# Kernel tuning notes

Hardware: AMD Instinct MI355X
Metric: run time of the kernel (lower is better)

Reference implementation:

```python
import jax, jax.numpy as jnp
import numpy as np

N_NODES = 100000
N_EDGES = 1600000
D = 32
N_GRAPHS = 128


def setup_inputs() -> dict:
    key = jax.random.key(0)
    ks = jax.random.split(key, 6)
    feats = jax.random.normal(ks[0], (N_NODES, D), dtype=jnp.float32)
    src = jax.random.randint(ks[1], (N_EDGES,), 0, N_NODES, dtype=jnp.int32)
    dst = jax.random.randint(ks[2], (N_EDGES,), 0, N_NODES, dtype=jnp.int32)
    graph_ids = jnp.sort(jax.random.randint(ks[3], (N_NODES,), 0, N_GRAPHS, dtype=jnp.int32))
    # Linear weights (torch nn.Linear: y = x @ W.T + b); store as [in, out] here
    W1 = jax.random.normal(ks[4], (D, D), dtype=jnp.float32) * (1.0 / np.sqrt(D))
    b1 = jnp.zeros((D,), dtype=jnp.float32)
    W2 = jax.random.normal(ks[5], (D, D), dtype=jnp.float32) * (1.0 / np.sqrt(D))
    b2 = jnp.zeros((D,), dtype=jnp.float32)
    return {"feats": feats, "src": src, "dst": dst, "graph_ids": graph_ids,
            "W1": W1, "b1": b1, "W2": W2, "b2": b2}


def _gin_conv(x, src, dst, W, b):
    # DGL GINConv, aggregator 'sum', eps=0 (default, non-learnable):
    # h_v = Linear(x_v + sum_{u in N(v)} x_u)
    agg = jax.ops.segment_sum(x[src], dst, num_segments=N_NODES)
    return (x + agg) @ W + b


def reference(feats, src, dst, graph_ids, W1, b1, W2, b2):
    h = _gin_conv(feats, src, dst, W1, b1)          # conv1
    h = jax.nn.relu(h)                               # F.relu
    h = _gin_conv(h, src, dst, W2, b2)               # conv2
    # SumPooling: sum node features per graph -> [N_GRAPHS, D]
    return jax.ops.segment_sum(h, graph_ids, num_segments=N_GRAPHS)
```

## Files before the change

### kernel.cpp

```cpp
#include <hip/hip_runtime.h>
#include <hip/hip_bf16.h>
#include <hip/hip_fp16.h>

#define N_NODES 100000
#define N_EDGES 1600000
#define D 32
#define N_GRAPHS 128

#define WIN 128
#define NWINS ((N_NODES + WIN - 1) / WIN)
#define CAP 2560
#define NODES_PER_WAVE 8

__global__ void bin_kernel(const int* __restrict__ src,
                           const int* __restrict__ dst,
                           int* __restrict__ gfill,
                           int* __restrict__ ebuf) {
    __shared__ int lhist[NWINS];
    __shared__ int lbase[NWINS];
    const int tid = threadIdx.x;
    const int per = (N_EDGES + gridDim.x - 1) / gridDim.x;
    const int e0 = blockIdx.x * per;
    const int e1 = (e0 + per < N_EDGES) ? e0 + per : N_EDGES;

    for (int b = tid; b < NWINS; b += blockDim.x) lhist[b] = 0;
    __syncthreads();
    for (int e = e0 + tid; e < e1; e += blockDim.x)
        atomicAdd(&lhist[dst[e] >> 7], 1);
    __syncthreads();
    for (int b = tid; b < NWINS; b += blockDim.x) {
        int c = lhist[b];
        lbase[b] = c ? atomicAdd(&gfill[b], c) : 0;
        lhist[b] = 0;
    }
    __syncthreads();
    for (int e = e0 + tid; e < e1; e += blockDim.x) {
        int d = dst[e];
        int bn = d >> 7;
        int r = atomicAdd(&lhist[bn], 1);
        int off = lbase[bn] + r;
        if (off < CAP) ebuf[bn * CAP + off] = ((d & (WIN - 1)) << 17) | src[e];
    }
}

__global__ void wscan_kernel(const int* __restrict__ gfill, int* __restrict__ wbase) {
    __shared__ int s[1024];
    const int t = threadIdx.x;
    int v = (t < NWINS) ? gfill[t] : 0;
    s[t] = v;
    __syncthreads();
    for (int off = 1; off < 1024; off <<= 1) {
        int a = (t >= off) ? s[t - off] : 0;
        __syncthreads();
        s[t] += a;
        __syncthreads();
    }
    if (t < NWINS) wbase[t] = s[t] - v;
    if (t == NWINS - 1) wbase[NWINS] = s[t];
}

__global__ void csr_local_kernel(const int* __restrict__ ebuf,
                                 const int* __restrict__ wbase,
                                 int* __restrict__ esrc,
                                 int* __restrict__ rend,
                                 int* __restrict__ deg) {
    __shared__ int pk[CAP];
    __shared__ int ssrc[CAP];
    __shared__ int hs[WIN];
    __shared__ int hcnt[WIN];
    __shared__ int cur[WIN];
    const int tid = threadIdx.x;
    const int w = blockIdx.x;
    const int base_out = wbase[w];
    int cnt = wbase[w + 1] - base_out;
    if (cnt > CAP) cnt = CAP;
    const int n0 = w * WIN;

    for (int i = tid; i < cnt; i += 256) pk[i] = ebuf[w * CAP + i];
    if (tid < WIN) hcnt[tid] = 0;
    __syncthreads();
    for (int i = tid; i < cnt; i += 256) atomicAdd(&hcnt[pk[i] >> 17], 1);
    __syncthreads();
    if (tid < WIN) hs[tid] = hcnt[tid];
    __syncthreads();
    for (int off = 1; off < WIN; off <<= 1) {
        int a = 0;
        if (tid < WIN && tid >= off) a = hs[tid - off];
        __syncthreads();
        if (tid < WIN) hs[tid] += a;
        __syncthreads();
    }
    if (tid < WIN) {
        const int incl = hs[tid];
        const int c = hcnt[tid];
        cur[tid] = incl - c;
        const int n = n0 + tid;
        if (n < N_NODES) { rend[n] = base_out + incl; deg[n] = c; }
    }
    __syncthreads();
    for (int i = tid; i < cnt; i += 256) {
        const int p = pk[i];
        const int pos = atomicAdd(&cur[p >> 17], 1);
        ssrc[pos] = p & 0x1FFFF;
    }
    __syncthreads();
    for (int i = tid; i < cnt; i += 256) esrc[base_out + i] = ssrc[i];
}

__device__ __forceinline__ unsigned pkh2(float a, float b) {
    __half2 h = __floats2half2_rn(a, b);
    return *reinterpret_cast<unsigned*>(&h);
}
__device__ __forceinline__ unsigned hadd2u(unsigned a, unsigned b) {
    __half2 ha = *reinterpret_cast<__half2*>(&a);
    __half2 hb = *reinterpret_cast<__half2*>(&b);
    __half2 r = __hadd2(ha, hb);
    return *reinterpret_cast<unsigned*>(&r);
}
__device__ __forceinline__ float lo2f(unsigned u) { return __low2float(*reinterpret_cast<__half2*>(&u)); }
__device__ __forceinline__ float hi2f(unsigned u) { return __high2float(*reinterpret_cast<__half2*>(&u)); }

__global__ void f32_to_f16_kernel(const float* __restrict__ in, uint4* __restrict__ out) {
    const int i = blockIdx.x * blockDim.x + threadIdx.x;
    if (i >= N_NODES * D / 8) return;
    const float4* p = reinterpret_cast<const float4*>(in) + (size_t)i * 2;
    const float4 v0 = p[0], v1 = p[1];
    uint4 o;
    o.x = pkh2(v0.x, v0.y); o.y = pkh2(v0.z, v0.w);
    o.z = pkh2(v1.x, v1.y); o.w = pkh2(v1.z, v1.w);
    out[i] = o;
}

#define PK_ADD(g) do { \
    acc01 = hadd2u(acc01, (g).x); acc23 = hadd2u(acc23, (g).y); \
    acc45 = hadd2u(acc45, (g).z); acc67 = hadd2u(acc67, (g).w); } while (0)

template <bool RELU, bool POOL>
__global__ void gin_layer_kernel(const uint4* __restrict__ xh,
                                 const int* __restrict__ esrc,
                                 const int* __restrict__ rend,
                                 const int* __restrict__ deg,
                                 const float* __restrict__ W,
                                 const float* __restrict__ bias,
                                 const int* __restrict__ graph_ids,
                                 float* __restrict__ outf,
                                 uint2* __restrict__ outh) {
    const int lane = threadIdx.x & 63;
    const int fq = lane & 3;
    const int es = lane >> 2;
    const int og = lane & 7;
    const int ig = lane >> 3;

    float w[4][4];
#pragma unroll
    for (int k = 0; k < 4; ++k) {
        const float4 t = *reinterpret_cast<const float4*>(&W[(ig * 4 + k) * D + og * 4]);
        w[k][0] = t.x; w[k][1] = t.y; w[k][2] = t.z; w[k][3] = t.w;
    }
    const float4 bv = *reinterpret_cast<const float4*>(&bias[og * 4]);

    const int wid = blockIdx.x * (blockDim.x >> 6) + (threadIdx.x >> 6);
    const int v0 = wid * NODES_PER_WAVE;
    if (v0 >= N_NODES) return;
    const int v1 = (v0 + NODES_PER_WAVE < N_NODES) ? v0 + NODES_PER_WAVE : N_NODES;

    float p0 = 0.f, p1 = 0.f, p2 = 0.f, p3 = 0.f;
    int cur_g = POOL ? graph_ids[v0] : 0;

    for (int v = v0; v < v1; ++v) {
        const int end = rend[v];
        int e = end - deg[v];

        unsigned acc01 = 0u, acc23 = 0u, acc45 = 0u, acc67 = 0u;
        if (es == 0) {
            const uint4 sv = xh[(size_t)v * 4 + fq];
            PK_ADD(sv);
        }

        for (; e + 32 <= end; e += 32) {
            const int r0 = esrc[e + es];
            const int r1 = esrc[e + 16 + es];
            const uint4 g0 = xh[(size_t)r0 * 4 + fq];
            const uint4 g1 = xh[(size_t)r1 * 4 + fq];
            PK_ADD(g0); PK_ADD(g1);
        }
        if (e + 16 <= end) {
            const int r0 = esrc[e + es];
            const uint4 g0 = xh[(size_t)r0 * 4 + fq];
            PK_ADD(g0);
            e += 16;
        }
        const int rem = end - e;
        if (es < rem) {
            const int r0 = esrc[e + es];
            const uint4 g0 = xh[(size_t)r0 * 4 + fq];
            PK_ADD(g0);
        }

#pragma unroll
        for (int off = 4; off <= 32; off <<= 1) {
            acc01 = hadd2u(acc01, (unsigned)__shfl_xor((int)acc01, off));
            acc23 = hadd2u(acc23, (unsigned)__shfl_xor((int)acc23, off));
            acc45 = hadd2u(acc45, (unsigned)__shfl_xor((int)acc45, off));
            acc67 = hadd2u(acc67, (unsigned)__shfl_xor((int)acc67, off));
        }

        const int s = ig >> 1;
        const int hi = ig & 1;
        const unsigned u0 = (unsigned)__shfl((int)acc01, s);
        const unsigned u1 = (unsigned)__shfl((int)acc23, s);
        const unsigned u2 = (unsigned)__shfl((int)acc45, s);
        const unsigned u3 = (unsigned)__shfl((int)acc67, s);
        const unsigned ua = hi ? u2 : u0;
        const unsigned ub = hi ? u3 : u1;
        const float q0 = lo2f(ua), q1 = hi2f(ua), q2 = lo2f(ub), q3 = hi2f(ub);

        float y0 = q0 * w[0][0] + q1 * w[1][0] + q2 * w[2][0] + q3 * w[3][0];
        float y1 = q0 * w[0][1] + q1 * w[1][1] + q2 * w[2][1] + q3 * w[3][1];
        float y2 = q0 * w[0][2] + q1 * w[1][2] + q2 * w[2][2] + q3 * w[3][2];
        float y3 = q0 * w[0][3] + q1 * w[1][3] + q2 * w[2][3] + q3 * w[3][3];

#pragma unroll
        for (int off = 8; off <= 32; off <<= 1) {
            y0 += __shfl_xor(y0, off); y1 += __shfl_xor(y1, off);
            y2 += __shfl_xor(y2, off); y3 += __shfl_xor(y3, off);
        }
        y0 += bv.x; y1 += bv.y; y2 += bv.z; y3 += bv.w;
        if (RELU) {
            y0 = fmaxf(y0, 0.f); y1 = fmaxf(y1, 0.f); y2 = fmaxf(y2, 0.f); y3 = fmaxf(y3, 0.f);
        }

        if (POOL) {
            const int g = graph_ids[v];
            if (g != cur_g) {
                if (ig == 0) {
                    atomicAdd(&outf[cur_g * D + og * 4 + 0], p0);
                    atomicAdd(&outf[cur_g * D + og * 4 + 1], p1);
                    atomicAdd(&outf[cur_g * D + og * 4 + 2], p2);
                    atomicAdd(&outf[cur_g * D + og * 4 + 3], p3);
                }
                p0 = p1 = p2 = p3 = 0.f;
                cur_g = g;
            }
            p0 += y0; p1 += y1; p2 += y2; p3 += y3;
        } else if (ig == 0) {
            uint2 o; o.x = pkh2(y0, y1); o.y = pkh2(y2, y3);
            outh[(size_t)v * 8 + og] = o;
        }
    }
    if (POOL && ig == 0) {
        atomicAdd(&outf[cur_g * D + og * 4 + 0], p0);
        atomicAdd(&outf[cur_g * D + og * 4 + 1], p1);
        atomicAdd(&outf[cur_g * D + og * 4 + 2], p2);
        atomicAdd(&outf[cur_g * D + og * 4 + 3], p3);
    }
}

extern "C" void kernel_launch(void* const* d_in, const int* in_sizes, int n_in,
                              void* d_out, int out_size, void* d_ws, size_t ws_size,
                              hipStream_t stream) {
    const float* feats = (const float*)d_in[0];
    const int* src = (const int*)d_in[1];
    const int* dst = (const int*)d_in[2];
    const int* graph_ids = (const int*)d_in[3];
    const float* W1 = (const float*)d_in[4];
    const float* b1 = (const float*)d_in[5];
    const float* W2 = (const float*)d_in[6];
    const float* b2 = (const float*)d_in[7];
    float* out = (float*)d_out;

    int* gfill = (int*)d_ws;
    int* wbase = gfill + 1024;
    int* ebuf  = wbase + 1024;
    int* esrc  = ebuf + (size_t)NWINS * CAP;
    int* rend  = esrc + N_EDGES;
    int* deg   = rend + N_NODES;
    unsigned* xh = (unsigned*)(deg + N_NODES);
    unsigned* hh = xh + (size_t)N_NODES * (D / 2);

    const int total_waves = (N_NODES + NODES_PER_WAVE - 1) / NODES_PER_WAVE;
    const int layer_blocks = (total_waves + 3) / 4;

    hipMemsetAsync(gfill, 0, 1024 * sizeof(int), stream);
    bin_kernel<<<256, 512, 0, stream>>>(src, dst, gfill, ebuf);
    wscan_kernel<<<1, 1024, 0, stream>>>(gfill, wbase);
    csr_local_kernel<<<NWINS, 256, 0, stream>>>(ebuf, wbase, esrc, rend, deg);

    f32_to_f16_kernel<<<(N_NODES * D / 8 + 255) / 256, 256, 0, stream>>>(
        feats, (uint4*)xh);

    gin_layer_kernel<true, false><<<layer_blocks, 256, 0, stream>>>(
        (const uint4*)xh, esrc, rend, deg, W1, b1, graph_ids, nullptr, (uint2*)hh);

    hipMemsetAsync(out, 0, (size_t)out_size * sizeof(float), stream);
    gin_layer_kernel<false, true><<<layer_blocks, 256, 0, stream>>>(
        (const uint4*)hh, esrc, rend, deg, W2, b2, graph_ids, out, nullptr);
}
```

Baseline: 145.3 us.

## Software-pipeline neighbor gathers across nodes in GIN layer kernel

Restructures the per-wave node loop into a fully unrolled software pipeline. Edge indices for node n+2 and the feature gathers for node n+1 are issued while node n is reduced and multiplied by the weights. Per-node rend/deg/graph_id are loaded once per wave and broadcast by shuffle, and the first 32 edges are covered by prefetched registers with a tail loop for higher degrees. This hides gather latency at the cost of more live registers, and it assumes N_NODES divides evenly by the nodes per wave times waves per block.

Result: slower. 151.9 us (+4.5%).

```diff
diff --git a/kernel.cpp b/kernel.cpp
--- a/kernel.cpp
+++ b/kernel.cpp
@@ -10,7 +10,7 @@
 #define WIN 128
 #define NWINS ((N_NODES + WIN - 1) / WIN)
 #define CAP 2560
-#define NODES_PER_WAVE 8
+#define NPW 8
 
 __global__ void bin_kernel(const int* __restrict__ src,
                            const int* __restrict__ dst,
@@ -136,15 +136,16 @@
     acc45 = hadd2u(acc45, (g).z); acc67 = hadd2u(acc67, (g).w); } while (0)
 
 template <bool RELU, bool POOL>
-__global__ void gin_layer_kernel(const uint4* __restrict__ xh,
-                                 const int* __restrict__ esrc,
-                                 const int* __restrict__ rend,
-                                 const int* __restrict__ deg,
-                                 const float* __restrict__ W,
-                                 const float* __restrict__ bias,
-                                 const int* __restrict__ graph_ids,
-                                 float* __restrict__ outf,
-                                 uint2* __restrict__ outh) {
+__global__ void __launch_bounds__(256)
+gin_layer_kernel(const uint4* __restrict__ xh,
+                 const int* __restrict__ esrc,
+                 const int* __restrict__ rend,
+                 const int* __restrict__ deg,
+                 const float* __restrict__ W,
+                 const float* __restrict__ bias,
+                 const int* __restrict__ graph_ids,
+                 float* __restrict__ outf,
+                 uint2* __restrict__ outh) {
     const int lane = threadIdx.x & 63;
     const int fq = lane & 3;
     const int es = lane >> 2;
@@ -159,42 +160,66 @@
     }
     const float4 bv = *reinterpret_cast<const float4*>(&bias[og * 4]);
 
-    const int wid = blockIdx.x * (blockDim.x >> 6) + (threadIdx.x >> 6);
-    const int v0 = wid * NODES_PER_WAVE;
+    const int wid = blockIdx.x * 4 + (threadIdx.x >> 6);
+    const int v0 = wid * NPW;
     if (v0 >= N_NODES) return;
-    const int v1 = (v0 + NODES_PER_WAVE < N_NODES) ? v0 + NODES_PER_WAVE : N_NODES;
+
+    const int vv = v0 + (lane & 7);
+    const int rend_v = rend[vv];
+    const int deg_v = deg[vv];
+    const int gid_v = POOL ? graph_ids[vv] : 0;
+
+    const uint4 Z = {0u, 0u, 0u, 0u};
+    uint4 GA, GB, SV, GA2, GB2, SV2;
+    int ia_nxt, ib_nxt, ia_fut, ib_fut;
+
+    {
+        const int Dm = __shfl(deg_v, 0);
+        const int Sm = __shfl(rend_v, 0) - Dm;
+        const int t0 = (es < Dm) ? esrc[Sm + es] : -1;
+        const int t1 = (16 + es < Dm) ? esrc[Sm + 16 + es] : -1;
+        GA = (t0 >= 0) ? xh[(size_t)t0 * 4 + fq] : Z;
+        GB = (t1 >= 0) ? xh[(size_t)t1 * 4 + fq] : Z;
+        SV = (es == 0) ? xh[(size_t)v0 * 4 + fq] : Z;
+    }
+    {
+        const int Dm = __shfl(deg_v, 1);
+        const int Sm = __shfl(rend_v, 1) - Dm;
+        ia_nxt = (es < Dm) ? esrc[Sm + es] : -1;
+        ib_nxt = (16 + es < Dm) ? esrc[Sm + 16 + es] : -1;
+    }
 
     float p0 = 0.f, p1 = 0.f, p2 = 0.f, p3 = 0.f;
-    int cur_g = POOL ? graph_ids[v0] : 0;
-
-    for (int v = v0; v < v1; ++v) {
-        const int end = rend[v];
-        int e = end - deg[v];
-
+    int cur_g = POOL ? __shfl(gid_v, 0) : 0;
+
+#pragma unroll
+    for (int n = 0; n < NPW; ++n) {
+        if (n + 2 < NPW) {
+            const int Dm = __shfl(deg_v, n + 2);
+            const int Sm = __shfl(rend_v, n + 2) - Dm;
+            ia_fut = (es < Dm) ? esrc[Sm + es] : -1;
+            ib_fut = (16 + es < Dm) ? esrc[Sm + 16 + es] : -1;
+        } else { ia_fut = -1; ib_fut = -1; }
+
+        if (n + 1 < NPW) {
+            GA2 = (ia_nxt >= 0) ? xh[(size_t)ia_nxt * 4 + fq] : Z;
+            GB2 = (ib_nxt >= 0) ? xh[(size_t)ib_nxt * 4 + fq] : Z;
+            SV2 = (es == 0) ? xh[(size_t)(v0 + n + 1) * 4 + fq] : Z;
+        } else { GA2 = Z; GB2 = Z; SV2 = Z; }
+
+        const int Dn_ = __shfl(deg_v, n);
+        const int Sn_ = __shfl(rend_v, n) - Dn_;
         unsigned acc01 = 0u, acc23 = 0u, acc45 = 0u, acc67 = 0u;
-        if (es == 0) {
-            const uint4 sv = xh[(size_t)v * 4 + fq];
-            PK_ADD(sv);
-        }
-
-        for (; e + 32 <= end; e += 32) {
-            const int r0 = esrc[e + es];
-            const int r1 = esrc[e + 16 + es];
-            const uint4 g0 = xh[(size_t)r0 * 4 + fq];
-            const uint4 g1 = xh[(size_t)r1 * 4 + fq];
-            PK_ADD(g0); PK_ADD(g1);
-        }
-        if (e + 16 <= end) {
-            const int r0 = esrc[e + es];
-            const uint4 g0 = xh[(size_t)r0 * 4 + fq];
-            PK_ADD(g0);
-            e += 16;
-        }
-        const int rem = end - e;
-        if (es < rem) {
-            const int r0 = esrc[e + es];
-            const uint4 g0 = xh[(size_t)r0 * 4 + fq];
-            PK_ADD(g0);
+        PK_ADD(SV); PK_ADD(GA); PK_ADD(GB);
+
+        const int endn = Sn_ + Dn_;
+        for (int e = Sn_ + 32; e < endn; e += 16) {
+            const int r = e + es;
+            if (r < endn) {
+                const int s0 = esrc[r];
+                const uint4 G = xh[(size_t)s0 * 4 + fq];
+                PK_ADD(G);
+            }
         }
 
 #pragma unroll
@@ -231,8 +256,8 @@
         }
 
         if (POOL) {
-            const int g = graph_ids[v];
-            if (g != cur_g) {
+            const int gg = __shfl(gid_v, n);
+            if (gg != cur_g) {
                 if (ig == 0) {
                     atomicAdd(&outf[cur_g * D + og * 4 + 0], p0);
                     atomicAdd(&outf[cur_g * D + og * 4 + 1], p1);
@@ -240,13 +265,16 @@
                     atomicAdd(&outf[cur_g * D + og * 4 + 3], p3);
                 }
                 p0 = p1 = p2 = p3 = 0.f;
-                cur_g = g;
+                cur_g = gg;
             }
             p0 += y0; p1 += y1; p2 += y2; p3 += y3;
         } else if (ig == 0) {
             uint2 o; o.x = pkh2(y0, y1); o.y = pkh2(y2, y3);
-            outh[(size_t)v * 8 + og] = o;
-        }
+            outh[(size_t)(v0 + n) * 8 + og] = o;
+        }
+
+        GA = GA2; GB = GB2; SV = SV2;
+        ia_nxt = ia_fut; ib_nxt = ib_fut;
     }
     if (POOL && ig == 0) {
         atomicAdd(&outf[cur_g * D + og * 4 + 0], p0);
@@ -278,8 +306,8 @@
     unsigned* xh = (unsigned*)(deg + N_NODES);
     unsigned* hh = xh + (size_t)N_NODES * (D / 2);
 
-    const int total_waves = (N_NODES + NODES_PER_WAVE - 1) / NODES_PER_WAVE;
-    const int layer_blocks = (total_waves + 3) / 4;
+    const int total_waves = N_NODES / NPW;
+    const int layer_blocks = total_waves / 4;
 
     hipMemsetAsync(gfill, 0, 1024 * sizeof(int), stream);
     bin_kernel<<<256, 512, 0, stream>>>(src, dst, gfill, ebuf);
```
